# Kernel optimization log

Hardware: AMD Instinct MI355X
Metric: run time of the kernel (lower is better)

## Reference

```python
import jax, jax.numpy as jnp
import numpy as np
from jax import lax

B, S, D_IN = 4, 4096, 1024
D_FAST, D_SLOW = 512, 512
Z_BIAS_FAST, Z_BIAS_SLOW = 2.0, -2.0


def _binop(q_i, q_j):
    a_i, b_i = q_i
    a_j, b_j = q_j
    return (a_i * a_j, a_j * b_i + b_j)


def parallel_scan(a, b):
    # h_t = a_t * h_{t-1} + b_t along seq axis (axis=1)
    _, h = lax.associative_scan(_binop, (a, b), axis=1)
    return h


def setup_inputs() -> dict:
    key = jax.random.key(0)
    ks = jax.random.split(key, 6)
    scale = 0.02
    x = jax.random.normal(ks[0], (B, S, D_IN), dtype=jnp.float32)
    W_zf = jax.random.normal(ks[1], (D_IN, D_FAST), dtype=jnp.float32) * scale
    b_zf = jnp.full((D_FAST,), Z_BIAS_FAST, dtype=jnp.float32)
    W_hf = jax.random.normal(ks[2], (D_IN, D_FAST), dtype=jnp.float32) * scale
    b_hf = jnp.zeros((D_FAST,), dtype=jnp.float32)
    W_zs = jax.random.normal(ks[3], (D_IN, D_SLOW), dtype=jnp.float32) * scale
    b_zs = jnp.full((D_SLOW,), Z_BIAS_SLOW, dtype=jnp.float32)
    W_hs = jax.random.normal(ks[4], (D_IN, D_SLOW), dtype=jnp.float32) * scale
    b_hs = jnp.zeros((D_SLOW,), dtype=jnp.float32)
    W_g = jax.random.normal(ks[5], (D_FAST + D_SLOW, D_FAST + D_SLOW), dtype=jnp.float32) * scale
    b_g = jnp.zeros((D_FAST + D_SLOW,), dtype=jnp.float32)
    return {"x": x, "W_zf": W_zf, "b_zf": b_zf, "W_hf": W_hf, "b_hf": b_hf,
            "W_zs": W_zs, "b_zs": b_zs, "W_hs": W_hs, "b_hs": b_hs,
            "W_g": W_g, "b_g": b_g}


def reference(x, W_zf, b_zf, W_hf, b_hf, W_zs, b_zs, W_hs, b_hs, W_g, b_g):
    # Fast compartment (coupling='output' => slow branch sees raw x)
    z_fast = jax.nn.sigmoid(jnp.einsum('bsd,df->bsf', x, W_zf) + b_zf)
    h_tilde_fast = jnp.einsum('bsd,df->bsf', x, W_hf) + b_hf
    h_fast = parallel_scan(1.0 - z_fast, z_fast * h_tilde_fast)

    # Slow compartment
    z_slow = jax.nn.sigmoid(jnp.einsum('bsd,df->bsf', x, W_zs) + b_zs)
    h_tilde_slow = jnp.einsum('bsd,df->bsf', x, W_hs) + b_hs
    h_slow = parallel_scan(1.0 - z_slow, z_slow * h_tilde_slow)

    h_combined = jnp.concatenate([h_fast, h_slow], axis=-1)  # (B, S, D_FAST+D_SLOW)
    gate = jax.nn.sigmoid(jnp.einsum('bsc,cd->bsd', h_combined, W_g) + b_g)
    return gate * h_combined
```

## Files before the change

### kernel.cpp

```cpp
#include <hip/hip_runtime.h>

#define BB 4
#define SS 4096
#define DIN 1024
#define DH 1024
#define PN 2048
#define MM (BB*SS)
#define NC 64
#define CL 64

typedef unsigned short ushort_t;
typedef __attribute__((ext_vector_type(8))) short bf16x8;
typedef __attribute__((ext_vector_type(4))) float f32x4;
typedef __attribute__((ext_vector_type(4))) unsigned short u16x4;

__device__ inline float bf2f(ushort_t u) {
    union { float f; unsigned int i; } v; v.i = ((unsigned int)u) << 16; return v.f;
}
__device__ inline ushort_t f2bf(float f) {
    union { float f; unsigned int i; } v; v.f = f;
    unsigned int r = v.i + 0x7fffu + ((v.i >> 16) & 1u);
    return (ushort_t)(r >> 16);
}
__device__ inline float sigmoidf_(float x) { return 1.0f / (1.0f + __expf(-x)); }

__device__ inline void load_lds16(const void* g, void* l) {
    __builtin_amdgcn_global_load_lds(
        (const __attribute__((address_space(1))) void*)g,
        (__attribute__((address_space(3))) void*)l, 16, 0, 0);
}

__global__ void zero_out_kernel(float* out, int n) {
    int i = blockIdx.x * 256 + threadIdx.x;
    if (i < n) out[i] = 0.0f;
}

#define PREP_NBLK 17160
__global__ __launch_bounds__(256) void prep_kernel(
    const float* __restrict__ x,
    const float* __restrict__ Wzf, const float* __restrict__ Wzs,
    const float* __restrict__ Whf, const float* __restrict__ Whs,
    const float* __restrict__ Wg,
    const float* __restrict__ bzf, const float* __restrict__ bzs,
    const float* __restrict__ bhf, const float* __restrict__ bhs,
    ushort_t* __restrict__ WcatT, ushort_t* __restrict__ WgT,
    ushort_t* __restrict__ Xb, float* __restrict__ bcat)
{
    __shared__ ushort_t tile[64][65];
    const int bx = blockIdx.x, tid = threadIdx.x;

    if (bx < 768) {
        const float* src; ushort_t* dst; int srcN, t;
        if (bx < 512) {
            int wi = bx >> 7; t = bx & 127; srcN = 512;
            const float* S[4] = {Wzf, Wzs, Whf, Whs};
            src = S[wi];
            dst = WcatT + (size_t)(wi * 512) * DIN;
        } else {
            t = bx - 512; srcN = 1024; src = Wg; dst = WgT;
        }
        const int k0 = (t & 15) * 64, n0 = (t >> 4) * 64;
        const int tx = tid & 63, ty = tid >> 6;
        #pragma unroll
        for (int i = ty; i < 64; i += 4)
            tile[i][tx] = f2bf(src[(size_t)(k0 + i) * srcN + n0 + tx]);
        __syncthreads();
        #pragma unroll
        for (int i = ty; i < 64; i += 4)
            dst[(size_t)(n0 + i) * DIN + k0 + tx] = tile[tx][i];
    } else if (bx < 17152) {
        size_t i = ((size_t)(bx - 768) * 256 + tid) * 4;
        float4 v = *(const float4*)(x + i);
        u16x4 o;
        o.x = f2bf(v.x); o.y = f2bf(v.y); o.z = f2bf(v.z); o.w = f2bf(v.w);
        *(u16x4*)(Xb + i) = o;
    } else {
        int i = (bx - 17152) * 256 + tid;
        float v = (i < 512) ? bzf[i] : (i < 1024) ? bzs[i - 512]
                : (i < 1536) ? bhf[i - 1024] : bhs[i - 1536];
        bcat[i] = v;
    }
}

#define VM4 asm volatile("s_waitcnt vmcnt(4)" ::: "memory")

#define STG_A(b, h, kt) { \
    _Pragma("unroll") \
    for (int j = 0; j < 2; j++) { \
        int c = wave * 2 + j; \
        load_lds16(Ablk + (size_t)((h) * 128 + c * 8) * lda + (kt) * 64 + laneAOff, \
                   &As[(b) * 16384 + (h) * 8192 + c * 512]); \
    } }

#define STG_B(b, h, kt) { \
    _Pragma("unroll") \
    for (int j = 0; j < 2; j++) { \
        int c = wave * 2 + j; \
        load_lds16(Bblk + (size_t)((h) * 128 + c * 8) * K + (kt) * 64 + laneBOff, \
                   &Bs[(b) * 16384 + (h) * 8192 + c * 512]); \
    } }

#define PHASE(b, qm, qn, STAGE, TAIL) { \
    bf16x8 af[4][2], bq[2][2]; \
    _Pragma("unroll") \
    for (int mt = 0; mt < 4; mt++) { \
        _Pragma("unroll") \
        for (int kh = 0; kh < 2; kh++) { \
            int r = (qm) * 128 + wm * 64 + mt * 16 + lrow; \
            af[mt][kh] = *(const bf16x8*)&As[(b) * 16384 + r * 64 + (((kh * 4 + kgrp) ^ (lrow & 7)) * 8)]; \
        } } \
    _Pragma("unroll") \
    for (int nt = 0; nt < 2; nt++) { \
        _Pragma("unroll") \
        for (int kh = 0; kh < 2; kh++) { \
            int r = (qn) * 128 + wn * 32 + nt * 16 + lrow; \
            bq[nt][kh] = *(const bf16x8*)&Bs[(b) * 16384 + r * 64 + (((kh * 4 + kgrp) ^ (lrow & 7)) * 8)]; \
        } } \
    STAGE; \
    asm volatile("s_barrier" ::: "memory"); \
    __builtin_amdgcn_s_setprio(1); \
    _Pragma("unroll") \
    for (int mt = 0; mt < 4; mt++) { \
        _Pragma("unroll") \
        for (int nt = 0; nt < 2; nt++) { \
            acc[qm][qn][mt][nt] = __builtin_amdgcn_mfma_f32_16x16x32_bf16( \
                af[mt][0], bq[nt][0], acc[qm][qn][mt][nt], 0, 0, 0); \
            acc[qm][qn][mt][nt] = __builtin_amdgcn_mfma_f32_16x16x32_bf16( \
                af[mt][1], bq[nt][1], acc[qm][qn][mt][nt], 0, 0, 0); \
        } } \
    __builtin_amdgcn_s_setprio(0); \
    TAIL; \
    asm volatile("s_barrier" ::: "memory"); \
  }

template <int EPI, int NB>
__global__ __launch_bounds__(512, 2) void gemm_kernel(
    const ushort_t* __restrict__ A, const ushort_t* __restrict__ Bt,
    int K, int lda,
    const float* __restrict__ bias,
    ushort_t* __restrict__ Zarr, ushort_t* __restrict__ Harr,
    const float* __restrict__ bg, const ushort_t* __restrict__ Hbf,
    float* __restrict__ Out)
{
    __shared__ alignas(16) ushort_t As[2 * 256 * 64];
    __shared__ alignas(16) ushort_t Bs[2 * 256 * 64];

    const int tid  = threadIdx.x;
    const int lane = tid & 63;
    const int wave = tid >> 6;
    const int wm   = wave & 1;
    const int wn   = wave >> 1;
    const int lrow = lane & 15;
    const int kgrp = lane >> 4;

    const int id  = blockIdx.x;
    const int xcd = id & 7;
    const int s   = id >> 3;
    const int mBase = (xcd + 8 * (s / NB)) * 256;
    const int nBase = (s % NB) * 256;

    f32x4 acc[2][2][4][2] = {};

    const ushort_t* Ablk = A  + (size_t)mBase * lda;
    const ushort_t* Bblk = Bt + (size_t)nBase * K;
    const int laneAOff = (lane >> 3) * lda + (((lane & 7) ^ (lane >> 3)) * 8);
    const int laneBOff = (lane >> 3) * K   + (((lane & 7) ^ (lane >> 3)) * 8);

    const int NKT = K >> 6;
    const int NIT = NKT >> 1;

    STG_A(0, 0, 0); STG_B(0, 0, 0); STG_A(0, 1, 0); STG_B(0, 1, 0);
    STG_A(1, 0, 1); STG_B(1, 0, 1);
    VM4;
    asm volatile("s_barrier" ::: "memory");

    for (int i = 0; i < NIT; i++) {
        const int kt1  = 2 * i + 1;
        const int ktn0 = (2 * i + 2) & (NKT - 1);
        const int ktn1 = (2 * i + 3) & (NKT - 1);
        PHASE(0, 0, 0, STG_A(1, 1, kt1),  );
        PHASE(0, 0, 1, STG_B(1, 1, kt1),  );
        PHASE(0, 1, 0, STG_A(0, 0, ktn0), );
        PHASE(0, 1, 1, STG_B(0, 0, ktn0), VM4);
        PHASE(1, 0, 0, STG_A(0, 1, ktn0), );
        PHASE(1, 0, 1, STG_B(0, 1, ktn0), );
        PHASE(1, 1, 0, STG_A(1, 0, ktn1), );
        PHASE(1, 1, 1, STG_B(1, 0, ktn1), VM4);
    }

    const int rquad = (lane >> 4) * 4;

    if (EPI == 0) {
        const bool isz = (nBase < DH);
        ushort_t* Dst  = isz ? Zarr : Harr;
        const int csub = isz ? 0 : DH;
        #pragma unroll
        for (int qm = 0; qm < 2; qm++)
        #pragma unroll
        for (int qn = 0; qn < 2; qn++)
        #pragma unroll
        for (int nt = 0; nt < 2; nt++) {
            int col  = nBase + qn * 128 + wn * 32 + nt * 16 + lrow;
            float bv = bias[col];
            int dcol = col - csub;
            #pragma unroll
            for (int mt = 0; mt < 4; mt++) {
                int row = mBase + qm * 128 + wm * 64 + mt * 16 + rquad;
                ushort_t* p = Dst + (size_t)row * DH + dcol;
                #pragma unroll
                for (int r = 0; r < 4; r++) {
                    float v = acc[qm][qn][mt][nt][r] + bv;
                    if (isz) v = sigmoidf_(v);
                    p[(size_t)r * DH] = f2bf(v);
                }
            }
        }
    } else {
        #pragma unroll
        for (int qm = 0; qm < 2; qm++)
        #pragma unroll
        for (int qn = 0; qn < 2; qn++)
        #pragma unroll
        for (int nt = 0; nt < 2; nt++) {
            int col  = nBase + qn * 128 + wn * 32 + nt * 16 + lrow;
            float bv = bg[col];
            #pragma unroll
            for (int mt = 0; mt < 4; mt++) {
                int row = mBase + qm * 128 + wm * 64 + mt * 16 + rquad;
                #pragma unroll
                for (int r = 0; r < 4; r++) {
                    float g = sigmoidf_(acc[qm][qn][mt][nt][r] + bv);
                    float h = bf2f(Hbf[(size_t)(row + r) * DH + col]);
                    Out[(size_t)(row + r) * DH + col] = g * h;
                }
            }
        }
    }
}

__global__ __launch_bounds__(256) void scan_chunk_agg(
    const ushort_t* __restrict__ Zarr, const ushort_t* __restrict__ Harr,
    float* __restrict__ Agg, float* __restrict__ Bagg)
{
    const int c4    = threadIdx.x * 4;
    const int chunk = blockIdx.x;
    const int b     = blockIdx.y;
    const size_t s0 = ((size_t)b * SS + (size_t)chunk * CL) * DH + c4;
    const ushort_t* Zp = Zarr + s0;
    const ushort_t* Hp = Harr + s0;

    float A0 = 1.0f, A1 = 1.0f, A2 = 1.0f, A3 = 1.0f;
    float B0 = 0.0f, B1 = 0.0f, B2 = 0.0f, B3 = 0.0f;
    #pragma unroll 8
    for (int t = 0; t < CL; t++) {
        u16x4 zv = *(const u16x4*)(Zp + (size_t)t * DH);
        u16x4 hv = *(const u16x4*)(Hp + (size_t)t * DH);
        float z0 = bf2f(zv.x), z1 = bf2f(zv.y), z2 = bf2f(zv.z), z3 = bf2f(zv.w);
        float h0 = bf2f(hv.x), h1 = bf2f(hv.y), h2 = bf2f(hv.z), h3 = bf2f(hv.w);
        A0 *= 1.0f - z0;  B0 = (1.0f - z0) * B0 + z0 * h0;
        A1 *= 1.0f - z1;  B1 = (1.0f - z1) * B1 + z1 * h1;
        A2 *= 1.0f - z2;  B2 = (1.0f - z2) * B2 + z2 * h2;
        A3 *= 1.0f - z3;  B3 = (1.0f - z3) * B3 + z3 * h3;
    }
    const size_t idx = ((size_t)(b * NC + chunk)) * DH + c4;
    *(float4*)(Agg  + idx) = make_float4(A0, A1, A2, A3);
    *(float4*)(Bagg + idx) = make_float4(B0, B1, B2, B3);
}

__global__ void scan_carry(const float* __restrict__ Agg, const float* __restrict__ Bagg,
                           float* __restrict__ Hinit)
{
    const int i = blockIdx.x * 256 + threadIdx.x;
    const int b = i >> 10, c = i & 1023;
    float h = 0.0f;
    for (int j = 0; j < NC; j++) {
        const size_t idx = ((size_t)(b * NC + j)) * DH + c;
        Hinit[idx] = h;
        h = Agg[idx] * h + Bagg[idx];
    }
}

__global__ __launch_bounds__(256) void scan_apply(
    const ushort_t* __restrict__ Zarr, ushort_t* Harr, const float* __restrict__ Hinit)
{
    const int c4    = threadIdx.x * 4;
    const int chunk = blockIdx.x;
    const int b     = blockIdx.y;
    const size_t s0 = ((size_t)b * SS + (size_t)chunk * CL) * DH + c4;
    const ushort_t* Zp = Zarr + s0;
    ushort_t*       Hp = Harr + s0;

    float4 hi = *(const float4*)(Hinit + ((size_t)(b * NC + chunk)) * DH + c4);
    float h0 = hi.x, h1 = hi.y, h2 = hi.z, h3 = hi.w;
    #pragma unroll 8
    for (int t = 0; t < CL; t++) {
        u16x4 zv = *(const u16x4*)(Zp + (size_t)t * DH);
        u16x4 hv = *(const u16x4*)(Hp + (size_t)t * DH);
        float z0 = bf2f(zv.x), z1 = bf2f(zv.y), z2 = bf2f(zv.z), z3 = bf2f(zv.w);
        float t0 = bf2f(hv.x), t1 = bf2f(hv.y), t2 = bf2f(hv.z), t3 = bf2f(hv.w);
        h0 = (1.0f - z0) * h0 + z0 * t0;
        h1 = (1.0f - z1) * h1 + z1 * t1;
        h2 = (1.0f - z2) * h2 + z2 * t2;
        h3 = (1.0f - z3) * h3 + z3 * t3;
        u16x4 o;
        o.x = f2bf(h0); o.y = f2bf(h1); o.z = f2bf(h2); o.w = f2bf(h3);
        *(u16x4*)(Hp + (size_t)t * DH) = o;
    }
}

extern "C" void kernel_launch(void* const* d_in, const int* in_sizes, int n_in,
                              void* d_out, int out_size, void* d_ws, size_t ws_size,
                              hipStream_t stream)
{
    const float* x   = (const float*)d_in[0];
    const float* Wzf = (const float*)d_in[1];
    const float* bzf = (const float*)d_in[2];
    const float* Whf = (const float*)d_in[3];
    const float* bhf = (const float*)d_in[4];
    const float* Wzs = (const float*)d_in[5];
    const float* bzs = (const float*)d_in[6];
    const float* Whs = (const float*)d_in[7];
    const float* bhs = (const float*)d_in[8];
    const float* Wg  = (const float*)d_in[9];
    const float* bg  = (const float*)d_in[10];

    const size_t NEED = (size_t)42 << 20;
    if (ws_size < NEED) {
        zero_out_kernel<<<(MM * DH + 255) / 256, 256, 0, stream>>>((float*)d_out, MM * DH);
        return;
    }

    char* ws = (char*)d_ws;
    ushort_t* WcatT = (ushort_t*)(ws);
    ushort_t* WgT   = (ushort_t*)(ws + ((size_t)4 << 20));
    float*    bcat  = (float*)   (ws + ((size_t)6 << 20));
    float*    Agg   = (float*)   (ws + ((size_t)6 << 20) + (64 << 10));
    float*    Bagg  = (float*)   (ws + ((size_t)7 << 20) + (64 << 10));
    float*    Hinit = (float*)   (ws + ((size_t)8 << 20) + (64 << 10));
    ushort_t* Harr  = (ushort_t*)(ws + ((size_t)10 << 20));

    ushort_t* Xb   = (ushort_t*)d_out;
    ushort_t* Zarr = Xb + (size_t)MM * DH;

    dim3 blk(256);

    prep_kernel<<<PREP_NBLK, blk, 0, stream>>>(
        x, Wzf, Wzs, Whf, Whs, Wg, bzf, bzs, bhf, bhs, WcatT, WgT, Xb, bcat);

    gemm_kernel<0, PN / 256><<<(MM / 256) * (PN / 256), dim3(512), 0, stream>>>(
        Xb, WcatT, DIN, DIN, bcat, Zarr, Harr, nullptr, nullptr, nullptr);

    scan_chunk_agg<<<dim3(NC, BB), blk, 0, stream>>>(Zarr, Harr, Agg, Bagg);
    scan_carry<<<16, 256, 0, stream>>>(Agg, Bagg, Hinit);
    scan_apply<<<dim3(NC, BB), blk, 0, stream>>>(Zarr, Harr, Hinit);

    gemm_kernel<1, DH / 256><<<(MM / 256) * (DH / 256), dim3(512), 0, stream>>>(
        Harr, WgT, DIN, DH, nullptr, nullptr, nullptr, bg, Harr,
        (float*)d_out);
}
```

Before: 338.2 us.

## Reuse LDS fragments across GEMM quadrant phases with explicit ds_read scheduling

Restructures the GEMM main loop so A and B fragments read from shared memory are kept in registers and reused across quadrant MFMA phases. This replaces reloading all operands for every phase and cuts LDS read traffic. Shared-memory reads now go through inline-asm ds_read_b128, with explicit lgkmcnt waits and sched_barrier fences, and the staging of the next k-tiles is re-interleaved to match. The cost is more live fragment registers and hand-placed waits, which could constrain the compiler's scheduling or add stalls.

Result: faster. 306.9 us (-9.3%).

```diff
diff --git a/kernel.cpp b/kernel.cpp
--- a/kernel.cpp
+++ b/kernel.cpp
@@ -28,6 +28,14 @@
     __builtin_amdgcn_global_load_lds(
         (const __attribute__((address_space(1))) void*)g,
         (__attribute__((address_space(3))) void*)l, 16, 0, 0);
+}
+
+__device__ __forceinline__ bf16x8 ds128(const ushort_t* p) {
+    bf16x8 r;
+    asm volatile("ds_read_b128 %0, %1"
+                 : "=v"(r)
+                 : "v"((const __attribute__((address_space(3))) ushort_t*)p));
+    return r;
 }
 
 __global__ void zero_out_kernel(float* out, int n) {
@@ -82,7 +90,9 @@
     }
 }
 
-#define VM4 asm volatile("s_waitcnt vmcnt(4)" ::: "memory")
+#define BARR __builtin_amdgcn_s_barrier()
+#define WAITK { asm volatile("s_waitcnt lgkmcnt(0)"); __builtin_amdgcn_sched_barrier(0); }
+#define VM4   { asm volatile("s_waitcnt vmcnt(4)");   __builtin_amdgcn_sched_barrier(0); }
 
 #define STG_A(b, h, kt) { \
     _Pragma("unroll") \
@@ -100,24 +110,25 @@
                    &Bs[(b) * 16384 + (h) * 8192 + c * 512]); \
     } }
 
-#define PHASE(b, qm, qn, STAGE, TAIL) { \
-    bf16x8 af[4][2], bq[2][2]; \
+#define LOADA(b, qm) { \
+    const ushort_t* p0 = &As[(b) * 16384 + (qm) * 8192 + arow0 + acol0]; \
+    const ushort_t* p1 = &As[(b) * 16384 + (qm) * 8192 + arow0 + acol1]; \
     _Pragma("unroll") \
     for (int mt = 0; mt < 4; mt++) { \
-        _Pragma("unroll") \
-        for (int kh = 0; kh < 2; kh++) { \
-            int r = (qm) * 128 + wm * 64 + mt * 16 + lrow; \
-            af[mt][kh] = *(const bf16x8*)&As[(b) * 16384 + r * 64 + (((kh * 4 + kgrp) ^ (lrow & 7)) * 8)]; \
-        } } \
+        af[mt][0] = ds128(p0 + mt * 1024); \
+        af[mt][1] = ds128(p1 + mt * 1024); \
+    } }
+
+#define LOADB(b, qn, bq) { \
+    const ushort_t* p0 = &Bs[(b) * 16384 + (qn) * 8192 + brow0 + acol0]; \
+    const ushort_t* p1 = &Bs[(b) * 16384 + (qn) * 8192 + brow0 + acol1]; \
     _Pragma("unroll") \
     for (int nt = 0; nt < 2; nt++) { \
-        _Pragma("unroll") \
-        for (int kh = 0; kh < 2; kh++) { \
-            int r = (qn) * 128 + wn * 32 + nt * 16 + lrow; \
-            bq[nt][kh] = *(const bf16x8*)&Bs[(b) * 16384 + r * 64 + (((kh * 4 + kgrp) ^ (lrow & 7)) * 8)]; \
-        } } \
-    STAGE; \
-    asm volatile("s_barrier" ::: "memory"); \
+        bq[nt][0] = ds128(p0 + nt * 1024); \
+        bq[nt][1] = ds128(p1 + nt * 1024); \
+    } }
+
+#define MFMA16(qm, qn, bq) { \
     __builtin_amdgcn_s_setprio(1); \
     _Pragma("unroll") \
     for (int mt = 0; mt < 4; mt++) { \
@@ -128,10 +139,7 @@
             acc[qm][qn][mt][nt] = __builtin_amdgcn_mfma_f32_16x16x32_bf16( \
                 af[mt][1], bq[nt][1], acc[qm][qn][mt][nt], 0, 0, 0); \
         } } \
-    __builtin_amdgcn_s_setprio(0); \
-    TAIL; \
-    asm volatile("s_barrier" ::: "memory"); \
-  }
+    __builtin_amdgcn_s_setprio(0); }
 
 template <int EPI, int NB>
 __global__ __launch_bounds__(512, 2) void gemm_kernel(
@@ -166,26 +174,43 @@
     const int laneAOff = (lane >> 3) * lda + (((lane & 7) ^ (lane >> 3)) * 8);
     const int laneBOff = (lane >> 3) * K   + (((lane & 7) ^ (lane >> 3)) * 8);
 
+    const int arow0 = (wm * 64 + lrow) * 64;
+    const int brow0 = (wn * 32 + lrow) * 64;
+    const int acol0 = ((kgrp    ) ^ (lrow & 7)) * 8;
+    const int acol1 = ((4 + kgrp) ^ (lrow & 7)) * 8;
+
     const int NKT = K >> 6;
     const int NIT = NKT >> 1;
+
+    bf16x8 af[4][2], bqA[2][2], bqB[2][2];
 
     STG_A(0, 0, 0); STG_B(0, 0, 0); STG_A(0, 1, 0); STG_B(0, 1, 0);
     STG_A(1, 0, 1); STG_B(1, 0, 1);
     VM4;
-    asm volatile("s_barrier" ::: "memory");
+    BARR;
 
     for (int i = 0; i < NIT; i++) {
         const int kt1  = 2 * i + 1;
         const int ktn0 = (2 * i + 2) & (NKT - 1);
         const int ktn1 = (2 * i + 3) & (NKT - 1);
-        PHASE(0, 0, 0, STG_A(1, 1, kt1),  );
-        PHASE(0, 0, 1, STG_B(1, 1, kt1),  );
-        PHASE(0, 1, 0, STG_A(0, 0, ktn0), );
-        PHASE(0, 1, 1, STG_B(0, 0, ktn0), VM4);
-        PHASE(1, 0, 0, STG_A(0, 1, ktn0), );
-        PHASE(1, 0, 1, STG_B(0, 1, ktn0), );
-        PHASE(1, 1, 0, STG_A(1, 0, ktn1), );
-        PHASE(1, 1, 1, STG_B(1, 0, ktn1), VM4);
+
+        LOADA(0, 0); LOADB(0, 0, bqA); STG_A(1, 1, kt1);
+        BARR; WAITK; MFMA16(0, 0, bqA); BARR;
+        LOADB(0, 1, bqB); STG_B(1, 1, kt1);
+        BARR; WAITK; MFMA16(0, 1, bqB); BARR;
+        LOADA(0, 1); STG_A(0, 0, ktn0);
+        BARR; WAITK; MFMA16(1, 1, bqB); BARR;
+        STG_B(0, 0, ktn0);
+        BARR; MFMA16(1, 0, bqA); VM4; BARR;
+
+        LOADA(1, 0); LOADB(1, 0, bqA); STG_B(0, 1, ktn0);
+        BARR; WAITK; MFMA16(0, 0, bqA); BARR;
+        LOADB(1, 1, bqB); STG_A(0, 1, ktn0);
+        BARR; WAITK; MFMA16(0, 1, bqB); BARR;
+        LOADA(1, 1); STG_A(1, 0, ktn1);
+        BARR; WAITK; MFMA16(1, 1, bqB); BARR;
+        STG_B(1, 0, ktn1);
+        BARR; MFMA16(1, 0, bqA); VM4; BARR;
     }
 
     const int rquad = (lane >> 4) * 4;
```
